# Kernel optimization log

Measured on AMD Instinct MI355X. Metric: run time of the kernel, lower is better.

## Reference

```python
import jax, jax.numpy as jnp
import numpy as np

EMBED_DIM = 768
NUM_HEADS = 12
HEAD_DIM = EMBED_DIM // NUM_HEADS
SCALING_FACTOR = 1.0
B, N = 1, 4096
K_PAIRS = 5


def setup_inputs() -> dict:
    key = jax.random.key(0)
    ks = jax.random.split(key, 10)
    s = EMBED_DIM ** -0.5
    return {
        "x": jax.random.normal(ks[0], (B, N, EMBED_DIM), dtype=jnp.float32),
        "similarity_matrix": jax.random.randint(ks[1], (N, K_PAIRS, 2), 0, N, dtype=jnp.int32),
        "Wq": jax.random.normal(ks[2], (EMBED_DIM, EMBED_DIM), dtype=jnp.float32) * s,
        "bq": jnp.zeros((EMBED_DIM,), dtype=jnp.float32),
        "Wk": jax.random.normal(ks[3], (EMBED_DIM, EMBED_DIM), dtype=jnp.float32) * s,
        "bk": jnp.zeros((EMBED_DIM,), dtype=jnp.float32),
        "Wv": jax.random.normal(ks[4], (EMBED_DIM, EMBED_DIM), dtype=jnp.float32) * s,
        "bv": jnp.zeros((EMBED_DIM,), dtype=jnp.float32),
        "Wo": jax.random.normal(ks[5], (EMBED_DIM, EMBED_DIM), dtype=jnp.float32) * s,
        "bo": jnp.zeros((EMBED_DIM,), dtype=jnp.float32),
    }


def _bias_matrix(similarity_matrix, n):
    # similarity_matrix: (N, K, 2) -> scatter-add SCALING_FACTOR at (i, idx)
    # for BOTH columns of every pair (duplicates accumulate, like +=).
    idx = similarity_matrix.reshape(n, -1)                 # (N, 2K)
    rows = jnp.broadcast_to(jnp.arange(n)[:, None], idx.shape)
    vals = jnp.where(idx < n, SCALING_FACTOR, 0.0).astype(jnp.float32)
    safe_idx = jnp.minimum(idx, n - 1)
    return jnp.zeros((n, n), dtype=jnp.float32).at[rows, safe_idx].add(vals)


def reference(x, similarity_matrix, Wq, bq, Wk, bk, Wv, bv, Wo, bo):
    b, n, c = x.shape
    h, d = NUM_HEADS, HEAD_DIM
    q = (x @ Wq.T + bq).reshape(b, n, h, d)
    k = (x @ Wk.T + bk).reshape(b, n, h, d)
    v = (x @ Wv.T + bv).reshape(b, n, h, d)
    scores = jnp.einsum("bihd,bjhd->bhij", q, k) * (d ** -0.5)  # (B,H,N,N)
    scores = scores + _bias_matrix(similarity_matrix, n)[None, None, :, :]
    attn = jax.nn.softmax(scores, axis=-1)
    out = jnp.einsum("bhij,bjhd->bihd", attn, v).reshape(b, n, c)
    return out @ Wo.T + bo
```

## Files before the change

kernel.cpp:

```cpp
#include <hip/hip_runtime.h>
#include <hip/hip_bf16.h>
#include <stdint.h>

#define N_TOK 4096
#define CDIM 768
#define NH 12
#define HD 64
#define SX (N_TOK * CDIM)
#define SW (CDIM * CDIM)

typedef __attribute__((ext_vector_type(8))) short bf16x8;
typedef __attribute__((ext_vector_type(4))) float f32x4;
typedef unsigned short ushort_t;
typedef unsigned int uint_t;

typedef const __attribute__((address_space(1))) void* as1_cvp;
typedef __attribute__((address_space(3))) void* as3_vp;
#define GLD16(g, s) __builtin_amdgcn_global_load_lds((as1_cvp)(g), (as3_vp)(s), 16, 0, 0)

__device__ inline ushort_t f2bf(float f) {
    union { float f; uint_t u; } c; c.f = f;
    uint_t u = (c.u + 0x7FFFu + ((c.u >> 16) & 1u)) >> 16;
    return (ushort_t)u;
}
__device__ inline uint_t pack_bf2(float a, float b) {
    union { __hip_bfloat162 v; uint_t u; } c;
    c.v = __float22bfloat162_rn(make_float2(a, b));
    return c.u;
}

__global__ __launch_bounds__(256) void convert_all(
    const float* __restrict__ x,
    const float* __restrict__ Wq, const float* __restrict__ Wk,
    const float* __restrict__ Wv, const float* __restrict__ Wo,
    const float* __restrict__ bq, const float* __restrict__ bk, const float* __restrict__ bv,
    ushort_t* __restrict__ xb, ushort_t* __restrict__ Wf,
    ushort_t* __restrict__ Wob, float* __restrict__ biasf)
{
    long i = ((long)blockIdx.x * 256 + threadIdx.x) * 4;
    const float* src; ushort_t* dst; long off;
    if (i < SX)               { src = x;  dst = xb;          off = i; }
    else if (i < SX + SW)     { src = Wq; dst = Wf;          off = i - SX; }
    else if (i < SX + 2*SW)   { src = Wk; dst = Wf + SW;     off = i - SX - SW; }
    else if (i < SX + 3*SW)   { src = Wv; dst = Wf + 2*SW;   off = i - SX - 2*SW; }
    else if (i < SX + 4*SW)   { src = Wo; dst = Wob;         off = i - SX - 3*SW; }
    else if (i < SX + 4*SW + 3*CDIM) {
        long b = i - (SX + 4*SW);
        const float* bs = (b < CDIM) ? bq + b : (b < 2*CDIM) ? bk + (b - CDIM) : bv + (b - 2*CDIM);
        *(float4*)(biasf + b) = *(const float4*)bs;
        return;
    } else return;
    float4 v4 = *(const float4*)(src + off);
    uint2 st = { pack_bf2(v4.x, v4.y), pack_bf2(v4.z, v4.w) };
    *(uint2*)(dst + off) = st;
}

__global__ __launch_bounds__(256) void gemm_qkv(
    const ushort_t* __restrict__ xb, const ushort_t* __restrict__ Wf,
    const float* __restrict__ biasf,
    ushort_t* __restrict__ q, ushort_t* __restrict__ k, ushort_t* __restrict__ vT)
{
    __shared__ __align__(16) ushort_t Asm[128 * 64];
    __shared__ __align__(16) ushort_t Bsm[64 * 64];
    const int tid = threadIdx.x;
    const int w = tid >> 6, lane = tid & 63;
    const int quad = lane >> 4, l16 = lane & 15;
    const int row0 = blockIdx.x * 128;
    const int col0 = blockIdx.y * 64;
    const int rw = w * 32;
    const int srow = lane >> 3;
    const int sc = ((lane & 7) ^ srow) * 8;
    const int swz = l16 & 7;
    const float C1 = 0.18033688011112042f;

    f32x4 acc[2][4];
#pragma unroll
    for (int a = 0; a < 2; a++)
#pragma unroll
        for (int b = 0; b < 4; b++) acc[a][b] = (f32x4){0.f, 0.f, 0.f, 0.f};

    for (int kc = 0; kc < CDIM; kc += 64) {
        __syncthreads();
#pragma unroll
        for (int c = 0; c < 4; c++) {
            int ra = w * 32 + c * 8;
            GLD16(xb + (size_t)(row0 + ra + srow) * CDIM + kc + sc, &Asm[ra * 64]);
        }
#pragma unroll
        for (int c = 0; c < 2; c++) {
            int rb_ = w * 16 + c * 8;
            GLD16(Wf + (size_t)(col0 + rb_ + srow) * CDIM + kc + sc, &Bsm[rb_ * 64]);
        }
        __syncthreads();
#pragma unroll
        for (int kk = 0; kk < 2; kk++) {
            const int po = ((kk * 4 + quad) ^ swz) * 8;
            bf16x8 af[2], bfr[4];
#pragma unroll
            for (int rb = 0; rb < 2; rb++)
                af[rb] = *(const bf16x8*)&Asm[(rw + rb * 16 + l16) * 64 + po];
#pragma unroll
            for (int cb = 0; cb < 4; cb++)
                bfr[cb] = *(const bf16x8*)&Bsm[(cb * 16 + l16) * 64 + po];
#pragma unroll
            for (int rb = 0; rb < 2; rb++)
#pragma unroll
                for (int cb = 0; cb < 4; cb++)
                    acc[rb][cb] = __builtin_amdgcn_mfma_f32_16x16x32_bf16(af[rb], bfr[cb], acc[rb][cb], 0, 0, 0);
        }
    }

    if (col0 < 2 * CDIM) {
        const bool isQ = (col0 < CDIM);
        ushort_t* dst = isQ ? q : k;
        const int jb0 = isQ ? col0 : col0 - CDIM;
        const float scale = isQ ? C1 : 1.0f;
#pragma unroll
        for (int cb = 0; cb < 4; cb++) {
            int j = jb0 + cb * 16 + l16;
            float bv_ = biasf[col0 + cb * 16 + l16];
#pragma unroll
            for (int rb = 0; rb < 2; rb++)
#pragma unroll
                for (int r = 0; r < 4; r++) {
                    int i = row0 + rw + rb * 16 + quad * 4 + r;
                    dst[(size_t)i * CDIM + j] = f2bf((acc[rb][cb][r] + bv_) * scale);
                }
        }
    } else {
        const int jv0 = col0 - 2 * CDIM;
        ushort_t* T = Asm;
        __syncthreads();
#pragma unroll
        for (int cb = 0; cb < 4; cb++) {
            int jl = cb * 16 + l16;
            float bv_ = biasf[col0 + jl];
#pragma unroll
            for (int rb = 0; rb < 2; rb++)
#pragma unroll
                for (int r = 0; r < 4; r++) {
                    int i = rw + rb * 16 + quad * 4 + r;
                    T[jl * 128 + (((i >> 3) ^ (jl & 7)) * 8) + (i & 7)] =
                        f2bf(acc[rb][cb][r] + bv_);
                }
        }
        __syncthreads();
#pragma unroll
        for (int p = 0; p < 4; p++) {
            int t = tid + p * 256, jl = t >> 4, i8 = t & 15;
            *(bf16x8*)(vT + (size_t)(jv0 + jl) * N_TOK + row0 + i8 * 8) =
                *(const bf16x8*)&T[jl * 128 + ((i8 ^ (jl & 7)) * 8)];
        }
    }
}

__global__ __launch_bounds__(256) void gemm_out(
    const ushort_t* __restrict__ A, const ushort_t* __restrict__ W,
    const float* __restrict__ bias, float* __restrict__ out)
{
    __shared__ __align__(16) ushort_t Asm[64 * 64];
    __shared__ __align__(16) ushort_t Bsm[64 * 64];
    const int tid = threadIdx.x;
    const int w = tid >> 6, lane = tid & 63;
    const int quad = lane >> 4, l16 = lane & 15;
    const int row0 = blockIdx.x * 64;
    const int col0 = blockIdx.y * 64;
    const int srow = lane >> 3;
    const int sc = ((lane & 7) ^ srow) * 8;
    const int swz = l16 & 7;

    f32x4 acc[4];
#pragma unroll
    for (int b = 0; b < 4; b++) acc[b] = (f32x4){0.f, 0.f, 0.f, 0.f};

    for (int kc = 0; kc < CDIM; kc += 64) {
        __syncthreads();
#pragma unroll
        for (int c = 0; c < 2; c++) {
            int ra = w * 16 + c * 8;
            GLD16(A + (size_t)(row0 + ra + srow) * CDIM + kc + sc, &Asm[ra * 64]);
            GLD16(W + (size_t)(col0 + ra + srow) * CDIM + kc + sc, &Bsm[ra * 64]);
        }
        __syncthreads();
#pragma unroll
        for (int kk = 0; kk < 2; kk++) {
            const int po = ((kk * 4 + quad) ^ swz) * 8;
            bf16x8 af = *(const bf16x8*)&Asm[(w * 16 + l16) * 64 + po];
#pragma unroll
            for (int cb = 0; cb < 4; cb++) {
                bf16x8 bfr = *(const bf16x8*)&Bsm[(cb * 16 + l16) * 64 + po];
                acc[cb] = __builtin_amdgcn_mfma_f32_16x16x32_bf16(af, bfr, acc[cb], 0, 0, 0);
            }
        }
    }
#pragma unroll
    for (int cb = 0; cb < 4; cb++) {
        int j = col0 + cb * 16 + l16;
        float bv_ = bias[j];
#pragma unroll
        for (int r = 0; r < 4; r++) {
            int i = row0 + w * 16 + quad * 4 + r;
            out[(size_t)i * CDIM + j] = acc[cb][r] + bv_;
        }
    }
}

__global__ __launch_bounds__(256, 6) void attn_kernel(
    const ushort_t* __restrict__ Q, const ushort_t* __restrict__ K,
    const ushort_t* __restrict__ VT, const int* __restrict__ sim,
    ushort_t* __restrict__ Oout)
{
    __shared__ __align__(16) ushort_t Ks[64 * 64];
    __shared__ __align__(16) ushort_t Vts[64 * 64];
    __shared__ __align__(16) ushort_t P2[32 * 64];
    __shared__ int ssim[32][12];
    __shared__ float psum[4][32];
    __shared__ float linvLDS[32];

    const int tid = threadIdx.x;
    const int wave = tid >> 6, lane = tid & 63;
    const int quad = lane >> 4, l16 = lane & 15;
    const int qbase = blockIdx.x * 32;
    const int hoff = blockIdx.y * HD;
    const float LOG2E = 1.4426950408889634f;

    const int srow = lane >> 3;
    const int sc = ((lane & 7) ^ srow) * 8;
    const int swz = l16 & 7;

    bf16x8 qf[2][2];
#pragma unroll
    for (int ib = 0; ib < 2; ib++)
#pragma unroll
        for (int kk = 0; kk < 2; kk++)
            qf[ib][kk] = *(const bf16x8*)(Q + (size_t)(qbase + ib * 16 + l16) * CDIM
                                          + hoff + kk * 32 + quad * 8);

    if (tid < 32) {
        int vb_[10];
        const int* sp = sim + (size_t)(qbase + tid) * 10;
#pragma unroll
        for (int e = 0; e < 10; e++) vb_[e] = sp[e];
#pragma unroll
        for (int round = 0; round < 10; round++)
#pragma unroll
            for (int i = (round & 1); i + 1 < 10; i += 2) {
                int a = vb_[i], b = vb_[i + 1];
                vb_[i] = min(a, b); vb_[i + 1] = max(a, b);
            }
#pragma unroll
        for (int e = 0; e < 10; e++) ssim[tid][e] = vb_[e];
        ssim[tid][10] = 0x7FFFFFFF;
        ssim[tid][11] = 0x7FFFFFFF;
    }
    __syncthreads();

    const ushort_t* kg0 = K + (size_t)(wave * 16 + srow) * CDIM + hoff + sc;
    const ushort_t* kg1 = K + (size_t)(wave * 16 + 8 + srow) * CDIM + hoff + sc;
    const ushort_t* vg0 = VT + (size_t)(hoff + wave * 16 + srow) * N_TOK + sc;
    const ushort_t* vg1 = VT + (size_t)(hoff + wave * 16 + 8 + srow) * N_TOK + sc;
    ushort_t* ksd0 = &Ks[(wave * 16) * 64];
    ushort_t* ksd1 = &Ks[(wave * 16 + 8) * 64];
    ushort_t* vtd0 = &Vts[(wave * 16) * 64];
    ushort_t* vtd1 = &Vts[(wave * 16 + 8) * 64];
    const ushort_t* kfp[2];
    const ushort_t* vfp[2];
#pragma unroll
    for (int kk = 0; kk < 2; kk++) {
        int po = ((kk * 4 + quad) ^ swz) * 8;
        kfp[kk] = &Ks[(wave * 16 + l16) * 64 + po];
        vfp[kk] = &Vts[(wave * 16 + l16) * 64 + po];
    }
    ushort_t* p2w[2];
    const ushort_t* p2r[2][2];
#pragma unroll
    for (int ib = 0; ib < 2; ib++) {
        int i = ib * 16 + l16;
        int cj = wave * 2 + (quad >> 1);
        p2w[ib] = &P2[i * 64 + (cj ^ (i & 7)) * 8 + (quad & 1) * 4];
#pragma unroll
        for (int kk = 0; kk < 2; kk++)
            p2r[kk][ib] = &P2[i * 64 + (((kk * 4 + quad) ^ (i & 7)) * 8)];
    }

    int curv[2], ptrv[2];
    float lsum[2] = { 0.f, 0.f };
    const int* srow0 = &ssim[l16][0];
    const int* srow1 = &ssim[16 + l16][0];
#pragma unroll
    for (int ib = 0; ib < 2; ib++) {
        ptrv[ib] = 0;
        curv[ib] = (ib ? srow1 : srow0)[0];
    }
    f32x4 Oacc[2];
#pragma unroll
    for (int a = 0; a < 2; a++) Oacc[a] = (f32x4){0.f, 0.f, 0.f, 0.f};

    for (int j0 = 0; j0 < N_TOK; j0 += 64) {
        __syncthreads();
        GLD16(kg0, ksd0); GLD16(kg1, ksd1);
        GLD16(vg0, vtd0); GLD16(vg1, vtd1);
        kg0 += 64 * CDIM; kg1 += 64 * CDIM;
        vg0 += 64;        vg1 += 64;
        __syncthreads();

        f32x4 sacc[2];
#pragma unroll
        for (int a = 0; a < 2; a++) sacc[a] = (f32x4){0.f, 0.f, 0.f, 0.f};
#pragma unroll
        for (int kk = 0; kk < 2; kk++) {
            bf16x8 ka = *(const bf16x8*)kfp[kk];
#pragma unroll
            for (int ib = 0; ib < 2; ib++)
                sacc[ib] = __builtin_amdgcn_mfma_f32_16x16x32_bf16(ka, qf[ib][kk], sacc[ib], 0, 0, 0);
        }

        const int jend = j0 + 64;
#pragma unroll
        for (int ib = 0; ib < 2; ib++) {
            int cu = curv[ib], pt = ptrv[ib];
            const int* sr = ib ? srow1 : srow0;
            while (cu < jend) {
                int c = cu - j0;
                if ((c >> 4) == wave && ((c >> 2) & 3) == quad) {
                    int rr = c & 3;
                    sacc[ib][0] += (rr == 0) ? LOG2E : 0.f;
                    sacc[ib][1] += (rr == 1) ? LOG2E : 0.f;
                    sacc[ib][2] += (rr == 2) ? LOG2E : 0.f;
                    sacc[ib][3] += (rr == 3) ? LOG2E : 0.f;
                }
                pt++;
                cu = sr[pt];
            }
            curv[ib] = cu; ptrv[ib] = pt;
        }

#pragma unroll
        for (int ib = 0; ib < 2; ib++) {
            float e0 = __builtin_amdgcn_exp2f(sacc[ib][0]);
            float e1 = __builtin_amdgcn_exp2f(sacc[ib][1]);
            float e2 = __builtin_amdgcn_exp2f(sacc[ib][2]);
            float e3 = __builtin_amdgcn_exp2f(sacc[ib][3]);
            lsum[ib] += (e0 + e1) + (e2 + e3);
            uint2 pk = { pack_bf2(e0, e1), pack_bf2(e2, e3) };
            *(uint2*)p2w[ib] = pk;
        }
        __syncthreads();

#pragma unroll
        for (int kk = 0; kk < 2; kk++) {
            bf16x8 vf = *(const bf16x8*)vfp[kk];
#pragma unroll
            for (int ib = 0; ib < 2; ib++) {
                bf16x8 pf = *(const bf16x8*)p2r[kk][ib];
                Oacc[ib] = __builtin_amdgcn_mfma_f32_16x16x32_bf16(pf, vf, Oacc[ib], 0, 0, 0);
            }
        }
    }

#pragma unroll
    for (int ib = 0; ib < 2; ib++) {
        float l = lsum[ib];
        l += __shfl_xor(l, 16, 64);
        l += __shfl_xor(l, 32, 64);
        if (quad == 0) psum[wave][ib * 16 + l16] = l;
    }
    __syncthreads();
    if (tid < 32)
        linvLDS[tid] = 1.0f / (psum[0][tid] + psum[1][tid] + psum[2][tid] + psum[3][tid]);
    __syncthreads();

    ushort_t (*Ov)[72] = (ushort_t(*)[72])Ks;
#pragma unroll
    for (int ib = 0; ib < 2; ib++)
#pragma unroll
        for (int r = 0; r < 4; r++) {
            int i = ib * 16 + quad * 4 + r;
            Ov[i][wave * 16 + l16] = f2bf(Oacc[ib][r] * linvLDS[i]);
        }
    __syncthreads();
    {
        int r = tid >> 3, c8 = tid & 7;
        *(bf16x8*)(Oout + (size_t)(qbase + r) * CDIM + hoff + c8 * 8) =
            *(const bf16x8*)&Ov[r][c8 * 8];
    }
}

extern "C" void kernel_launch(void* const* d_in, const int* in_sizes, int n_in,
                              void* d_out, int out_size, void* d_ws, size_t ws_size,
                              hipStream_t stream)
{
    const float* x   = (const float*)d_in[0];
    const int*   sim = (const int*)d_in[1];
    const float* Wq  = (const float*)d_in[2];
    const float* bq  = (const float*)d_in[3];
    const float* Wk  = (const float*)d_in[4];
    const float* bk  = (const float*)d_in[5];
    const float* Wv  = (const float*)d_in[6];
    const float* bv  = (const float*)d_in[7];
    const float* Wo  = (const float*)d_in[8];
    const float* bo  = (const float*)d_in[9];
    float* out = (float*)d_out;

    ushort_t* xb  = (ushort_t*)d_ws;
    ushort_t* q   = xb + SX;
    ushort_t* k   = q + SX;
    ushort_t* vT  = k + SX;
    ushort_t* Wf  = vT + SX;
    ushort_t* Wob = Wf + 3 * SW;
    float* biasf  = (float*)(Wob + SW);
    ushort_t* ao  = xb;

    dim3 blk(256);
    {
        long total4 = (long)(SX + 4 * SW + 3 * CDIM) / 4;
        int nb = (int)((total4 + 255) / 256);
        convert_all<<<nb, blk, 0, stream>>>(x, Wq, Wk, Wv, Wo, bq, bk, bv,
                                            xb, Wf, Wob, biasf);
    }
    {
        dim3 g(N_TOK / 128, (3 * CDIM) / 64);
        gemm_qkv<<<g, blk, 0, stream>>>(xb, Wf, biasf, q, k, vT);
    }
    {
        dim3 g(N_TOK / 32, NH);
        attn_kernel<<<g, blk, 0, stream>>>(q, k, vT, sim, ao);
    }
    {
        dim3 g(N_TOK / 64, CDIM / 64);
        gemm_out<<<g, blk, 0, stream>>>(ao, Wob, bo, out);
    }
}
```

Before: 244.0 us.

## Restructure attention kernel with 32x32 MFMA, double-buffered K/V, register-resident P

```diff
diff --git a/kernel.cpp b/kernel.cpp
--- a/kernel.cpp
+++ b/kernel.cpp
@@ -11,6 +11,7 @@
 
 typedef __attribute__((ext_vector_type(8))) short bf16x8;
 typedef __attribute__((ext_vector_type(4))) float f32x4;
+typedef __attribute__((ext_vector_type(16))) float f32x16;
 typedef unsigned short ushort_t;
 typedef unsigned int uint_t;
 
@@ -205,38 +206,41 @@
     }
 }
 
-__global__ __launch_bounds__(256, 6) void attn_kernel(
+__global__ __launch_bounds__(256, 3) void attn_kernel(
     const ushort_t* __restrict__ Q, const ushort_t* __restrict__ K,
     const ushort_t* __restrict__ VT, const int* __restrict__ sim,
     ushort_t* __restrict__ Oout)
 {
-    __shared__ __align__(16) ushort_t Ks[64 * 64];
-    __shared__ __align__(16) ushort_t Vts[64 * 64];
-    __shared__ __align__(16) ushort_t P2[32 * 64];
-    __shared__ int ssim[32][12];
-    __shared__ float psum[4][32];
-    __shared__ float linvLDS[32];
+    __shared__ __align__(16) ushort_t smem[16384];
+    __shared__ int ssim[64][12];
+    __shared__ float psum[128];
 
     const int tid = threadIdx.x;
-    const int wave = tid >> 6, lane = tid & 63;
-    const int quad = lane >> 4, l16 = lane & 15;
-    const int qbase = blockIdx.x * 32;
-    const int hoff = blockIdx.y * HD;
+    const int w = tid >> 6, lane = tid & 63;
+    const int hi = lane >> 5, l32 = lane & 31;
+    const int qs = w >> 1, jh = w & 1;
     const float LOG2E = 1.4426950408889634f;
+
+    const int lin = blockIdx.x;
+    const int g = (lin & 7) * 96 + (lin >> 3);
+    const int qbase = (g & 63) * 64;
+    const int hoff = (g >> 6) * HD;
 
     const int srow = lane >> 3;
     const int sc = ((lane & 7) ^ srow) * 8;
-    const int swz = l16 & 7;
-
-    bf16x8 qf[2][2];
-#pragma unroll
-    for (int ib = 0; ib < 2; ib++)
-#pragma unroll
-        for (int kk = 0; kk < 2; kk++)
-            qf[ib][kk] = *(const bf16x8*)(Q + (size_t)(qbase + ib * 16 + l16) * CDIM
-                                          + hoff + kk * 32 + quad * 8);
-
-    if (tid < 32) {
+    const ushort_t* kg0 = K + (size_t)(w * 16 + srow) * CDIM + hoff + sc;
+    const ushort_t* kg1 = kg0 + 8 * CDIM;
+    const ushort_t* vg0 = VT + (size_t)(hoff + w * 16 + srow) * N_TOK + sc;
+    const ushort_t* vg1 = vg0 + 8 * (size_t)N_TOK;
+    ushort_t* kda = &smem[(w * 16) * 64];
+    ushort_t* vda = &smem[8192 + (w * 16) * 64];
+
+#define STAGE(KD, VD) do { \
+    GLD16(kg0, (KD)); GLD16(kg1, (KD) + 512); \
+    GLD16(vg0, (VD)); GLD16(vg1, (VD) + 512); \
+    kg0 += 64 * CDIM; kg1 += 64 * CDIM; vg0 += 64; vg1 += 64; } while (0)
+
+    if (tid < 64) {
         int vb_[10];
         const int* sp = sim + (size_t)(qbase + tid) * 10;
 #pragma unroll
@@ -253,136 +257,152 @@
         ssim[tid][10] = 0x7FFFFFFF;
         ssim[tid][11] = 0x7FFFFFFF;
     }
+
+    bf16x8 qf[4];
+    {
+        const ushort_t* qp = Q + (size_t)(qbase + qs * 32 + l32) * CDIM + hoff + hi * 8;
+#pragma unroll
+        for (int kk = 0; kk < 4; kk++) qf[kk] = *(const bf16x8*)(qp + kk * 16);
+    }
+
+    const int swz = l32 & 7;
+    const ushort_t* kfp[4];
+#pragma unroll
+    for (int kk = 0; kk < 4; kk++)
+        kfp[kk] = &smem[(jh * 32 + l32) * 64 + (((kk * 2 + hi) ^ swz) * 8)];
+    const ushort_t* vfp[2][2];
+#pragma unroll
+    for (int db = 0; db < 2; db++)
+#pragma unroll
+        for (int k2 = 0; k2 < 2; k2++)
+            vfp[db][k2] = &smem[8192 + db * 2048 + l32 * 64 + (((jh * 4 + k2 * 2 + hi) ^ swz) * 8)];
+
+    STAGE(kda, vda);
     __syncthreads();
 
-    const ushort_t* kg0 = K + (size_t)(wave * 16 + srow) * CDIM + hoff + sc;
-    const ushort_t* kg1 = K + (size_t)(wave * 16 + 8 + srow) * CDIM + hoff + sc;
-    const ushort_t* vg0 = VT + (size_t)(hoff + wave * 16 + srow) * N_TOK + sc;
-    const ushort_t* vg1 = VT + (size_t)(hoff + wave * 16 + 8 + srow) * N_TOK + sc;
-    ushort_t* ksd0 = &Ks[(wave * 16) * 64];
-    ushort_t* ksd1 = &Ks[(wave * 16 + 8) * 64];
-    ushort_t* vtd0 = &Vts[(wave * 16) * 64];
-    ushort_t* vtd1 = &Vts[(wave * 16 + 8) * 64];
-    const ushort_t* kfp[2];
-    const ushort_t* vfp[2];
-#pragma unroll
-    for (int kk = 0; kk < 2; kk++) {
-        int po = ((kk * 4 + quad) ^ swz) * 8;
-        kfp[kk] = &Ks[(wave * 16 + l16) * 64 + po];
-        vfp[kk] = &Vts[(wave * 16 + l16) * 64 + po];
-    }
-    ushort_t* p2w[2];
-    const ushort_t* p2r[2][2];
-#pragma unroll
-    for (int ib = 0; ib < 2; ib++) {
-        int i = ib * 16 + l16;
-        int cj = wave * 2 + (quad >> 1);
-        p2w[ib] = &P2[i * 64 + (cj ^ (i & 7)) * 8 + (quad & 1) * 4];
-#pragma unroll
-        for (int kk = 0; kk < 2; kk++)
-            p2r[kk][ib] = &P2[i * 64 + (((kk * 4 + quad) ^ (i & 7)) * 8)];
-    }
-
-    int curv[2], ptrv[2];
-    float lsum[2] = { 0.f, 0.f };
-    const int* srow0 = &ssim[l16][0];
-    const int* srow1 = &ssim[16 + l16][0];
-#pragma unroll
-    for (int ib = 0; ib < 2; ib++) {
-        ptrv[ib] = 0;
-        curv[ib] = (ib ? srow1 : srow0)[0];
-    }
-    f32x4 Oacc[2];
-#pragma unroll
-    for (int a = 0; a < 2; a++) Oacc[a] = (f32x4){0.f, 0.f, 0.f, 0.f};
-
-    for (int j0 = 0; j0 < N_TOK; j0 += 64) {
-        __syncthreads();
-        GLD16(kg0, ksd0); GLD16(kg1, ksd1);
-        GLD16(vg0, vtd0); GLD16(vg1, vtd1);
-        kg0 += 64 * CDIM; kg1 += 64 * CDIM;
-        vg0 += 64;        vg1 += 64;
-        __syncthreads();
-
-        f32x4 sacc[2];
-#pragma unroll
-        for (int a = 0; a < 2; a++) sacc[a] = (f32x4){0.f, 0.f, 0.f, 0.f};
-#pragma unroll
-        for (int kk = 0; kk < 2; kk++) {
-            bf16x8 ka = *(const bf16x8*)kfp[kk];
-#pragma unroll
-            for (int ib = 0; ib < 2; ib++)
-                sacc[ib] = __builtin_amdgcn_mfma_f32_16x16x32_bf16(ka, qf[ib][kk], sacc[ib], 0, 0, 0);
-        }
-
-        const int jend = j0 + 64;
-#pragma unroll
-        for (int ib = 0; ib < 2; ib++) {
-            int cu = curv[ib], pt = ptrv[ib];
-            const int* sr = ib ? srow1 : srow0;
-            while (cu < jend) {
-                int c = cu - j0;
-                if ((c >> 4) == wave && ((c >> 2) & 3) == quad) {
-                    int rr = c & 3;
-                    sacc[ib][0] += (rr == 0) ? LOG2E : 0.f;
-                    sacc[ib][1] += (rr == 1) ? LOG2E : 0.f;
-                    sacc[ib][2] += (rr == 2) ? LOG2E : 0.f;
-                    sacc[ib][3] += (rr == 3) ? LOG2E : 0.f;
-                }
-                pt++;
-                cu = sr[pt];
-            }
-            curv[ib] = cu; ptrv[ib] = pt;
-        }
-
-#pragma unroll
-        for (int ib = 0; ib < 2; ib++) {
-            float e0 = __builtin_amdgcn_exp2f(sacc[ib][0]);
-            float e1 = __builtin_amdgcn_exp2f(sacc[ib][1]);
-            float e2 = __builtin_amdgcn_exp2f(sacc[ib][2]);
-            float e3 = __builtin_amdgcn_exp2f(sacc[ib][3]);
-            lsum[ib] += (e0 + e1) + (e2 + e3);
-            uint2 pk = { pack_bf2(e0, e1), pack_bf2(e2, e3) };
-            *(uint2*)p2w[ib] = pk;
-        }
-        __syncthreads();
-
-#pragma unroll
-        for (int kk = 0; kk < 2; kk++) {
-            bf16x8 vf = *(const bf16x8*)vfp[kk];
-#pragma unroll
-            for (int ib = 0; ib < 2; ib++) {
-                bf16x8 pf = *(const bf16x8*)p2r[kk][ib];
-                Oacc[ib] = __builtin_amdgcn_mfma_f32_16x16x32_bf16(pf, vf, Oacc[ib], 0, 0, 0);
-            }
-        }
-    }
-
-#pragma unroll
-    for (int ib = 0; ib < 2; ib++) {
-        float l = lsum[ib];
-        l += __shfl_xor(l, 16, 64);
-        l += __shfl_xor(l, 32, 64);
-        if (quad == 0) psum[wave][ib * 16 + l16] = l;
-    }
+    const int* srp = &ssim[qs * 32 + l32][0];
+    int pt = 0, cu = srp[0];
+    float lsum = 0.f;
+    f32x16 Oacc0 = {0.f,0.f,0.f,0.f,0.f,0.f,0.f,0.f,0.f,0.f,0.f,0.f,0.f,0.f,0.f,0.f};
+    f32x16 Oacc1 = {0.f,0.f,0.f,0.f,0.f,0.f,0.f,0.f,0.f,0.f,0.f,0.f,0.f,0.f,0.f,0.f};
+
+#define TILE_BODY(OFS, J0) do { \
+    f32x16 sacc = {0.f,0.f,0.f,0.f,0.f,0.f,0.f,0.f,0.f,0.f,0.f,0.f,0.f,0.f,0.f,0.f}; \
+    _Pragma("unroll") \
+    for (int kk = 0; kk < 4; kk++) { \
+        bf16x8 kf = *(const bf16x8*)(kfp[kk] + (OFS)); \
+        sacc = __builtin_amdgcn_mfma_f32_32x32x16_bf16(kf, qf[kk], sacc, 0, 0, 0); \
+    } \
+    { const int jend = (J0) + 64; \
+      const int cb = (J0) + jh * 32 + hi * 4; \
+      while (cu < jend) { \
+        int d = cu - cb; \
+        sacc[0]  += (d == 0)  ? LOG2E : 0.f; \
+        sacc[1]  += (d == 1)  ? LOG2E : 0.f; \
+        sacc[2]  += (d == 2)  ? LOG2E : 0.f; \
+        sacc[3]  += (d == 3)  ? LOG2E : 0.f; \
+        sacc[4]  += (d == 8)  ? LOG2E : 0.f; \
+        sacc[5]  += (d == 9)  ? LOG2E : 0.f; \
+        sacc[6]  += (d == 10) ? LOG2E : 0.f; \
+        sacc[7]  += (d == 11) ? LOG2E : 0.f; \
+        sacc[8]  += (d == 16) ? LOG2E : 0.f; \
+        sacc[9]  += (d == 17) ? LOG2E : 0.f; \
+        sacc[10] += (d == 18) ? LOG2E : 0.f; \
+        sacc[11] += (d == 19) ? LOG2E : 0.f; \
+        sacc[12] += (d == 24) ? LOG2E : 0.f; \
+        sacc[13] += (d == 25) ? LOG2E : 0.f; \
+        sacc[14] += (d == 26) ? LOG2E : 0.f; \
+        sacc[15] += (d == 27) ? LOG2E : 0.f; \
+        pt++; cu = srp[pt]; \
+      } } \
+    float e0  = __builtin_amdgcn_exp2f(sacc[0]); \
+    float e1  = __builtin_amdgcn_exp2f(sacc[1]); \
+    float e2  = __builtin_amdgcn_exp2f(sacc[2]); \
+    float e3  = __builtin_amdgcn_exp2f(sacc[3]); \
+    float e4  = __builtin_amdgcn_exp2f(sacc[4]); \
+    float e5  = __builtin_amdgcn_exp2f(sacc[5]); \
+    float e6  = __builtin_amdgcn_exp2f(sacc[6]); \
+    float e7  = __builtin_amdgcn_exp2f(sacc[7]); \
+    float e8  = __builtin_amdgcn_exp2f(sacc[8]); \
+    float e9  = __builtin_amdgcn_exp2f(sacc[9]); \
+    float e10 = __builtin_amdgcn_exp2f(sacc[10]); \
+    float e11 = __builtin_amdgcn_exp2f(sacc[11]); \
+    float e12 = __builtin_amdgcn_exp2f(sacc[12]); \
+    float e13 = __builtin_amdgcn_exp2f(sacc[13]); \
+    float e14 = __builtin_amdgcn_exp2f(sacc[14]); \
+    float e15 = __builtin_amdgcn_exp2f(sacc[15]); \
+    lsum += (((e0+e1)+(e2+e3)) + ((e4+e5)+(e6+e7))) \
+          + (((e8+e9)+(e10+e11)) + ((e12+e13)+(e14+e15))); \
+    uint_t A0 = pack_bf2(e0, e1),   C0 = pack_bf2(e2, e3); \
+    uint_t B0 = pack_bf2(e4, e5),   D0 = pack_bf2(e6, e7); \
+    uint_t A1 = pack_bf2(e8, e9),   C1_ = pack_bf2(e10, e11); \
+    uint_t B1 = pack_bf2(e12, e13), D1 = pack_bf2(e14, e15); \
+    asm("v_permlane32_swap_b32 %0, %1" : "+v"(A0), "+v"(B0)); \
+    asm("v_permlane32_swap_b32 %0, %1" : "+v"(C0), "+v"(D0)); \
+    asm("v_permlane32_swap_b32 %0, %1" : "+v"(A1), "+v"(B1)); \
+    asm("v_permlane32_swap_b32 %0, %1" : "+v"(C1_), "+v"(D1)); \
+    union { uint_t u[4]; bf16x8 v; } pa0_, pa1_; \
+    pa0_.u[0] = A0; pa0_.u[1] = C0; pa0_.u[2] = B0; pa0_.u[3] = D0; \
+    pa1_.u[0] = A1; pa1_.u[1] = C1_; pa1_.u[2] = B1; pa1_.u[3] = D1; \
+    { \
+        bf16x8 v00 = *(const bf16x8*)(vfp[0][0] + (OFS)); \
+        bf16x8 v01 = *(const bf16x8*)(vfp[0][1] + (OFS)); \
+        Oacc0 = __builtin_amdgcn_mfma_f32_32x32x16_bf16(pa0_.v, v00, Oacc0, 0, 0, 0); \
+        Oacc0 = __builtin_amdgcn_mfma_f32_32x32x16_bf16(pa1_.v, v01, Oacc0, 0, 0, 0); \
+        bf16x8 v10 = *(const bf16x8*)(vfp[1][0] + (OFS)); \
+        bf16x8 v11 = *(const bf16x8*)(vfp[1][1] + (OFS)); \
+        Oacc1 = __builtin_amdgcn_mfma_f32_32x32x16_bf16(pa0_.v, v10, Oacc1, 0, 0, 0); \
+        Oacc1 = __builtin_amdgcn_mfma_f32_32x32x16_bf16(pa1_.v, v11, Oacc1, 0, 0, 0); \
+    } \
+  } while (0)
+
+    for (int t = 0; t < 64; t += 2) {
+        STAGE(kda + 4096, vda + 4096);
+        TILE_BODY(0, t * 64);
+        __syncthreads();
+        if (t + 2 < 64) STAGE(kda, vda);
+        TILE_BODY(4096, (t + 1) * 64);
+        __syncthreads();
+    }
+#undef TILE_BODY
+#undef STAGE
+
+    float lt = lsum + __shfl_xor(lsum, 32, 64);
+    if (lane < 32) psum[qs * 64 + jh * 32 + l32] = lt;
+
+    float* Of = (float*)smem;
+#define OROWS(OACC, DB, OP) do { \
+    _Pragma("unroll") \
+    for (int r = 0; r < 16; r++) { \
+        int i_ = qs * 32 + (r & 3) + 8 * (r >> 2) + 4 * hi; \
+        Of[i_ * 66 + (DB) * 32 + l32] OP (OACC)[r]; \
+    } } while (0)
+
+    if (jh == 0) { OROWS(Oacc0, 0, =); OROWS(Oacc1, 1, =); }
     __syncthreads();
-    if (tid < 32)
-        linvLDS[tid] = 1.0f / (psum[0][tid] + psum[1][tid] + psum[2][tid] + psum[3][tid]);
+    if (jh == 1) { OROWS(Oacc0, 0, +=); OROWS(Oacc1, 1, +=); }
     __syncthreads();
-
-    ushort_t (*Ov)[72] = (ushort_t(*)[72])Ks;
-#pragma unroll
-    for (int ib = 0; ib < 2; ib++)
-#pragma unroll
-        for (int r = 0; r < 4; r++) {
-            int i = ib * 16 + quad * 4 + r;
-            Ov[i][wave * 16 + l16] = f2bf(Oacc[ib][r] * linvLDS[i]);
-        }
-    __syncthreads();
-    {
-        int r = tid >> 3, c8 = tid & 7;
-        *(bf16x8*)(Oout + (size_t)(qbase + r) * CDIM + hoff + c8 * 8) =
-            *(const bf16x8*)&Ov[r][c8 * 8];
+#undef OROWS
+
+    {
+        int row = tid >> 2, c0 = (tid & 3) * 16;
+        int li = row & 31, qr = row >> 5;
+        float inv = 1.0f / (psum[qr * 64 + li] + psum[qr * 64 + 32 + li]);
+        const float* rp = Of + row * 66 + c0;
+        uint_t w0 = pack_bf2(rp[0]  * inv, rp[1]  * inv);
+        uint_t w1 = pack_bf2(rp[2]  * inv, rp[3]  * inv);
+        uint_t w2 = pack_bf2(rp[4]  * inv, rp[5]  * inv);
+        uint_t w3 = pack_bf2(rp[6]  * inv, rp[7]  * inv);
+        uint_t w4 = pack_bf2(rp[8]  * inv, rp[9]  * inv);
+        uint_t w5 = pack_bf2(rp[10] * inv, rp[11] * inv);
+        uint_t w6 = pack_bf2(rp[12] * inv, rp[13] * inv);
+        uint_t w7 = pack_bf2(rp[14] * inv, rp[15] * inv);
+        union { uint_t u[4]; bf16x8 v; } oA, oB;
+        oA.u[0] = w0; oA.u[1] = w1; oA.u[2] = w2; oA.u[3] = w3;
+        oB.u[0] = w4; oB.u[1] = w5; oB.u[2] = w6; oB.u[3] = w7;
+        ushort_t* op = Oout + (size_t)(qbase + row) * CDIM + hoff + c0;
+        *(bf16x8*)op = oA.v;
+        *(bf16x8*)(op + 8) = oB.v;
     }
 }
 
@@ -423,7 +443,7 @@
         gemm_qkv<<<g, blk, 0, stream>>>(xb, Wf, biasf, q, k, vT);
     }
     {
-        dim3 g(N_TOK / 32, NH);
+        dim3 g((N_TOK / 64) * NH);
         attn_kernel<<<g, blk, 0, stream>>>(q, k, vT, sim, ao);
     }
     {
```

Result: faster. 205.8 us (-15.7%).
